# Kernel optimization log

Measured on AMD Instinct MI355X. Metric: run time of the kernel, lower is better.

## Reference

```python
import jax, jax.numpy as jnp
import numpy as np

N_E = 8192
E_DIM = 256
BETA = 0.25


def setup_inputs() -> dict:
    key = jax.random.key(0)
    k_z, k_w = jax.random.split(key)
    z = jax.random.normal(k_z, (32, E_DIM, 32, 32), dtype=jnp.float32)
    # nn.Embedding weight init: uniform(-1/n_e, 1/n_e)
    W = jax.random.uniform(k_w, (N_E, E_DIM), dtype=jnp.float32,
                           minval=-1.0 / N_E, maxval=1.0 / N_E)
    return {"z": z, "W": W}


def reference(z, W):
    B, C, H, Wd = z.shape
    beta = jnp.float32(BETA)
    z_nhwc = jnp.transpose(z, (0, 2, 3, 1))          # (B,H,W,C)
    zf = z_nhwc.reshape(-1, C)                       # (N,C)
    # squared-distance matrix (N, n_e)
    d = (jnp.sum(zf * zf, axis=1, keepdims=True)
         + jnp.sum(W * W, axis=1)
         - 2.0 * jnp.matmul(zf, W.T))
    idx = jnp.argmin(d, axis=1)                      # (N,)
    # one-hot @ W == gather
    z_q = W[idx].reshape(z_nhwc.shape)               # (B,H,W,C)
    loss = (jnp.mean((jax.lax.stop_gradient(z_q) - z_nhwc) ** 2)
            + beta * jnp.mean((z_q - jax.lax.stop_gradient(z_nhwc)) ** 2))
    # straight-through estimator
    z_q = z_nhwc + jax.lax.stop_gradient(z_q - z_nhwc)
    # codebook usage perplexity
    n = idx.shape[0]
    e_mean = jnp.zeros((N_E,), jnp.float32).at[idx].add(1.0) / n
    perplexity = jnp.exp(-jnp.sum(e_mean * jnp.log(e_mean + 1e-10)))
    z_q = jnp.transpose(z_q, (0, 3, 1, 2))           # back to (B,C,H,W)
    index = idx.reshape(B, H, Wd)
    return z_q, loss, index, perplexity
```

## Files before the change

kernel.cpp:

```cpp
#include <hip/hip_runtime.h>
#include <float.h>
#include <math.h>

#define OUT_LOSS 8388608
#define OUT_IDX  8388609
#define OUT_PERP 8421377

#define WS_ZH    0ull
#define WS_ZL    16777216ull
#define WS_ZT    0ull
#define WS_WH    33554432ull
#define WS_S     37748736ull
#define WS_B     37879808ull
#define WS_MAXW  37912576ull
#define WS_IDX   37912640ull
#define WS_HIST  38043712ull
#define WS_CAND  38076480ull
#define WS_FULL  38469696ull
#define WS_FKEY  38600768ull
#define WS_CNT   38862912ull
#define WS_LOSS  38862920ull
#define WS_WL    38866944ull

typedef short v8s __attribute__((ext_vector_type(8)));
typedef float v4f __attribute__((ext_vector_type(4)));

__device__ __forceinline__ unsigned short bf16rne(float f) {
  unsigned u = __float_as_uint(f);
  return (unsigned short)((u + 0x7FFFu + ((u >> 16) & 1u)) >> 16);
}
__device__ __forceinline__ float bf16tof(unsigned short h) {
  return __uint_as_float(((unsigned)h) << 16);
}

__device__ __forceinline__ void gl_lds16(const void* g, void* l) {
  __builtin_amdgcn_global_load_lds(
      (const __attribute__((address_space(1))) unsigned int*)g,
      (__attribute__((address_space(3))) unsigned int*)l, 16, 0, 0);
}

__global__ void k_zero(int* __restrict__ hist, unsigned long long* __restrict__ fkey,
                       int* __restrict__ cnt, double* __restrict__ loss,
                       unsigned* __restrict__ maxw) {
  const int i = blockIdx.x * 256 + threadIdx.x;
  if (i < 8192) hist[i] = 0;
  else if (i < 40960) fkey[i - 8192] = ~0ull;
  else if (i == 40960) cnt[0] = 0;
  else if (i == 40961) cnt[1] = 0;
  else if (i == 40962) *loss = 0.0;
  else if (i == 40963) *maxw = 0u;
}

__global__ __launch_bounds__(256) void k_split(const float* __restrict__ W,
                                               unsigned short* __restrict__ Wh,
                                               unsigned short* __restrict__ Wl) {
  const int u = blockIdx.x * 256 + threadIdx.x;
  const int kc = u >> 15, grp = (u >> 6) & 511, q = (u >> 4) & 3, col = u & 15;
  const int j = grp * 16 + col, k0 = kc * 32 + q * 8;
  const float4 w0 = *(const float4*)(W + (size_t)j * 256 + k0);
  const float4 w1 = *(const float4*)(W + (size_t)j * 256 + k0 + 4);
  const float wv[8] = {w0.x, w0.y, w0.z, w0.w, w1.x, w1.y, w1.z, w1.w};
  unsigned short h[8] __attribute__((aligned(16)));
  unsigned short l[8] __attribute__((aligned(16)));
#pragma unroll
  for (int i = 0; i < 8; ++i) {
    h[i] = bf16rne(wv[i]);
    l[i] = bf16rne(__fsub_rn(wv[i], bf16tof(h[i])));
  }
  *(uint4*)(Wh + (size_t)u * 8) = *(const uint4*)h;
  *(uint4*)(Wl + (size_t)u * 8) = *(const uint4*)l;
}

__global__ __launch_bounds__(256) void k_splitz(const float* __restrict__ z,
    unsigned short* __restrict__ Zh, unsigned short* __restrict__ Zl) {
  const int gt = blockIdx.x * 256 + threadIdx.x;
  const int kc = gt >> 15;
  const int n  = gt & 32767;
  const int b = n >> 10, p = n & 1023;
  const float* zp = z + (size_t)b * 262144 + (size_t)(kc * 32) * 1024 + p;
  unsigned short hh[32] __attribute__((aligned(16)));
  unsigned short ll[32] __attribute__((aligned(16)));
#pragma unroll
  for (int i = 0; i < 32; ++i) {
    const float v = zp[(size_t)i * 1024];
    const unsigned short h = bf16rne(v);
    hh[i] = h;
    ll[i] = bf16rne(__fsub_rn(v, bf16tof(h)));
  }
  const size_t o = (size_t)kc * 1048576 + (size_t)(n >> 4) * 512 + (size_t)(n & 15) * 8;
#pragma unroll
  for (int q = 0; q < 4; ++q) *(uint4*)(Zh + o + q * 128) = *(const uint4*)(hh + q * 8);
#pragma unroll
  for (int q = 0; q < 4; ++q) *(uint4*)(Zl + o + q * 128) = *(const uint4*)(ll + q * 8);
}

__global__ __launch_bounds__(256) void k_zt(const float* __restrict__ z,
                                            float* __restrict__ zT) {
  const int gt = blockIdx.x * 256 + threadIdx.x;
  const int kc = gt >> 15;
  const int n  = gt & 32767;
  const int b = n >> 10, p = n & 1023;
  const float* zp = z + (size_t)b * 262144 + (size_t)(kc * 32) * 1024 + p;
  float v[32] __attribute__((aligned(16)));
#pragma unroll
  for (int i = 0; i < 32; ++i) v[i] = zp[(size_t)i * 1024];
  float* dst = zT + (size_t)n * 256 + kc * 32;
#pragma unroll
  for (int j = 0; j < 8; ++j) *(float4*)(dst + j * 4) = *(const float4*)(v + j * 4);
}

__device__ __forceinline__ float np_sumsq256(const float* __restrict__ base,
                                             const int stride) {
  float h[2];
#pragma unroll
  for (int half = 0; half < 2; ++half) {
    const float* a = base + (size_t)(half * 128) * stride;
    float r[8];
#pragma unroll
    for (int k = 0; k < 8; ++k) { const float v = a[(size_t)k * stride]; r[k] = __fmul_rn(v, v); }
    for (int i = 8; i < 128; i += 8) {
#pragma unroll
      for (int k = 0; k < 8; ++k) {
        const float v = a[(size_t)(i + k) * stride];
        r[k] = __fadd_rn(r[k], __fmul_rn(v, v));
      }
    }
    h[half] = __fadd_rn(
        __fadd_rn(__fadd_rn(r[0], r[1]), __fadd_rn(r[2], r[3])),
        __fadd_rn(__fadd_rn(r[4], r[5]), __fadd_rn(r[6], r[7])));
  }
  return __fadd_rn(h[0], h[1]);
}

__global__ __launch_bounds__(256) void k_sz(const float* __restrict__ z,
                                            float* __restrict__ S) {
  const int n = blockIdx.x * 256 + threadIdx.x;
  S[n] = np_sumsq256(z + (size_t)(n >> 10) * 262144 + (n & 1023), 1024);
}

__global__ __launch_bounds__(256) void k_wsq(const float* __restrict__ W,
                                             float* __restrict__ B,
                                             unsigned* __restrict__ maxw) {
  const int j = blockIdx.x * 256 + threadIdx.x;
  const float b = np_sumsq256(W + (size_t)j * 256, 1);
  B[j] = b;
  atomicMax(maxw, __float_as_uint(b));
}

__device__ __forceinline__ void merge5(float& a1, int& ai1, float& a2, int& ai2,
                                       float& a3, float b1, int bi1, float b2,
                                       int bi2, float b3) {
  const bool t1 = (b1 < a1) || (b1 == a1 && bi1 < ai1);
  const float w2v = t1 ? b2 : a2; const int w2i = t1 ? bi2 : ai2;
  const float w3v = t1 ? b3 : a3;
  const float l1v = t1 ? a1 : b1; const int l1i = t1 ? ai1 : bi1;
  const float l2v = t1 ? a2 : b2;
  const float n1v = t1 ? b1 : a1; const int n1i = t1 ? bi1 : ai1;
  const bool t2 = (w2v < l1v) || (w2v == l1v && w2i < l1i);
  a1 = n1v; ai1 = n1i;
  a2 = t2 ? w2v : l1v; ai2 = t2 ? w2i : l1i;
  a3 = t2 ? fminf(w3v, l1v) : fminf(w2v, l2v);
}

#define AL_OFF   0
#define BH0_OFF  32768
#define BH1_OFF  65536
#define BL0_OFF  98304
#define BL1_OFF  131072
#define SC_OFF   32768
#define SMEM_SZ  163840
__global__ __launch_bounds__(512, 1) void k_main(
    const unsigned short* __restrict__ Zh, const unsigned short* __restrict__ Zl,
    const unsigned short* __restrict__ Wh, const unsigned short* __restrict__ Wl,
    const float* __restrict__ S, const float* __restrict__ B,
    const unsigned* __restrict__ maxw, int* __restrict__ idxb,
    int* __restrict__ cand, int* __restrict__ full, int* __restrict__ cnt) {
  extern __shared__ __align__(16) char smem[];
  const int t = threadIdx.x;
  const int w = t >> 6, lane = t & 63, col = lane & 15, q = lane >> 4;
  const int phalf = w >> 2, strip = w & 3;
  const int n0 = blockIdx.x << 6;

  float spx[8];
#pragma unroll
  for (int s = 0; s < 8; ++s)
    spx[s] = S[n0 + phalf * 32 + (s >> 2) * 16 + q * 4 + (s & 3)];

  v8s ah[8][2];
  const size_t abase = (size_t)(n0 >> 4) * 512 + (size_t)lane * 8;
#pragma unroll
  for (int kc = 0; kc < 8; ++kc)
#pragma unroll
    for (int pt = 0; pt < 2; ++pt)
      ah[kc][pt] = *(const v8s*)(Zh + (size_t)kc * 1048576 + abase
                                 + (size_t)(phalf * 2 + pt) * 512);

  {
    const size_t ab = (size_t)w * 1048576 + abase;
    char* dl = smem + AL_OFF + w * 4096;
#pragma unroll
    for (int i = 0; i < 4; ++i) gl_lds16(Zl + ab + (size_t)i * 512, dl + i * 1024);
  }
  {
    const size_t bb = (size_t)(w * 4) * 512 + (size_t)lane * 8;
#pragma unroll
    for (int i = 0; i < 4; ++i)
      gl_lds16(Wh + bb + (size_t)i * 512, smem + BH0_OFF + (w * 4 + i) * 1024);
#pragma unroll
    for (int i = 0; i < 4; ++i)
      gl_lds16(Wl + bb + (size_t)i * 512, smem + BL0_OFF + (w * 4 + i) * 1024);
  }
  __syncthreads();

  float m1[8], m2[8], m3[8]; int i1[8], i2[8];
#pragma unroll
  for (int s = 0; s < 8; ++s) {
    m1[s] = FLT_MAX; m2[s] = FLT_MAX; m3[s] = FLT_MAX;
    i1[s] = 0x7fffffff; i2[s] = 0x7fffffff;
  }

  v4f acc[2][8];
#pragma unroll
  for (int pt = 0; pt < 2; ++pt)
#pragma unroll
    for (int nt = 0; nt < 8; ++nt) acc[pt][nt] = (v4f){0.f, 0.f, 0.f, 0.f};

  for (int ct = 0; ct < 16; ++ct) {
#pragma unroll
    for (int kc = 0; kc < 8; ++kc) {
      const int it = ct * 8 + kc;
      if (it < 127) {
        const int nc = it + 1;
        const size_t cb = (size_t)(nc & 7) * 262144 + (size_t)(nc >> 3) * 16384
                        + (size_t)(w * 4) * 512 + (size_t)lane * 8;
        char* nh = smem + ((nc & 1) ? BH1_OFF : BH0_OFF) + (w * 4) * 1024;
        char* nl = smem + ((nc & 1) ? BL1_OFF : BL0_OFF) + (w * 4) * 1024;
#pragma unroll
        for (int i = 0; i < 4; ++i)
          gl_lds16(Wh + cb + (size_t)i * 512, nh + i * 1024);
#pragma unroll
        for (int i = 0; i < 4; ++i)
          gl_lds16(Wl + cb + (size_t)i * 512, nl + i * 1024);
      }
      const char* bhb = smem + ((it & 1) ? BH1_OFF : BH0_OFF);
      const char* blb = smem + ((it & 1) ? BL1_OFF : BL0_OFF);
      v8s al[2];
#pragma unroll
      for (int pt = 0; pt < 2; ++pt)
        al[pt] = *(const v8s*)(smem + AL_OFF + kc * 4096
                               + (phalf * 2 + pt) * 1024 + lane * 16);
#pragma unroll
      for (int nt = 0; nt < 8; ++nt) {
        const v8s bh = *(const v8s*)(bhb + (strip * 8 + nt) * 1024 + lane * 16);
        const v8s bl = *(const v8s*)(blb + (strip * 8 + nt) * 1024 + lane * 16);
#pragma unroll
        for (int pt = 0; pt < 2; ++pt) {
          acc[pt][nt] = __builtin_amdgcn_mfma_f32_16x16x32_bf16(ah[kc][pt], bh, acc[pt][nt], 0, 0, 0);
          acc[pt][nt] = __builtin_amdgcn_mfma_f32_16x16x32_bf16(al[pt], bh, acc[pt][nt], 0, 0, 0);
          acc[pt][nt] = __builtin_amdgcn_mfma_f32_16x16x32_bf16(ah[kc][pt], bl, acc[pt][nt], 0, 0, 0);
        }
      }
      __syncthreads();
      if (kc == 7) {
#pragma unroll
        for (int nt = 0; nt < 8; ++nt) {
          const int code = ct * 512 + strip * 128 + nt * 16 + col;
          const float bb = B[code];
#pragma unroll
          for (int pt = 0; pt < 2; ++pt) {
            const v4f a = acc[pt][nt];
#pragma unroll
            for (int r = 0; r < 4; ++r) {
              const int s = pt * 4 + r;
              const float d = __fsub_rn(__fadd_rn(spx[s], bb), __fmul_rn(2.f, a[r]));
              const bool c1 = (d < m1[s]);
              const bool c2 = (d < m2[s]);
              const bool c3 = (d < m3[s]);
              m3[s] = c2 ? m2[s] : (c3 ? d : m3[s]);
              m2[s] = c1 ? m1[s] : (c2 ? d : m2[s]);
              i2[s] = c1 ? i1[s] : (c2 ? code : i2[s]);
              m1[s] = c1 ? d : m1[s];
              i1[s] = c1 ? code : i1[s];
            }
          }
#pragma unroll
          for (int pt = 0; pt < 2; ++pt) acc[pt][nt] = (v4f){0.f, 0.f, 0.f, 0.f};
        }
      }
    }
  }

#pragma unroll
  for (int s = 0; s < 8; ++s) {
    for (int msk = 1; msk < 16; msk <<= 1) {
      const float b1 = __shfl_xor(m1[s], msk, 16);
      const int  bi1 = __shfl_xor(i1[s], msk, 16);
      const float b2 = __shfl_xor(m2[s], msk, 16);
      const int  bi2 = __shfl_xor(i2[s], msk, 16);
      const float b3 = __shfl_xor(m3[s], msk, 16);
      merge5(m1[s], i1[s], m2[s], i2[s], m3[s], b1, bi1, b2, bi2, b3);
    }
  }
  __syncthreads();
  float* sc = (float*)(smem + SC_OFF);
  if (col == 0) {
#pragma unroll
    for (int s = 0; s < 8; ++s) {
      const int px = phalf * 32 + (s >> 2) * 16 + q * 4 + (s & 3);
      const int base = (px * 4 + strip) * 5;
      sc[base]     = m1[s];
      sc[base + 1] = __int_as_float(i1[s]);
      sc[base + 2] = m2[s];
      sc[base + 3] = __int_as_float(i2[s]);
      sc[base + 4] = m3[s];
    }
  }
  __syncthreads();
  if (t < 64) {
    const int base0 = t * 20;
    float A1 = sc[base0], A2 = sc[base0 + 2], A3 = sc[base0 + 4];
    int AI1 = __float_as_int(sc[base0 + 1]), AI2 = __float_as_int(sc[base0 + 3]);
    for (int st = 1; st < 4; ++st) {
      const int base = base0 + st * 5;
      merge5(A1, AI1, A2, AI2, A3, sc[base], __float_as_int(sc[base + 1]),
             sc[base + 2], __float_as_int(sc[base + 3]), sc[base + 4]);
    }
    const int n = n0 + t;
    idxb[n] = AI1;
    const float nw = sqrtf(S[n]) * sqrtf(__uint_as_float(*maxw));
    const float win = 2.0f * (1.52587890625e-05f * nw + 1e-6f)
                    + 2.0f * ldexpf(1.0f, ilogbf(fmaxf(A1, 1e-30f)) - 23);
    if (A2 <= A1 + win) {
      if (A3 <= A1 + win) {
        const int p = atomicAdd(&cnt[1], 1);
        full[p] = n;
      } else {
        const int p = atomicAdd(&cnt[0], 1);
        cand[3 * p] = n; cand[3 * p + 1] = AI1; cand[3 * p + 2] = AI2;
      }
    }
  }
}

__global__ __launch_bounds__(256) void k_cand(const float* __restrict__ zT,
    const float* __restrict__ W, const float* __restrict__ S,
    const float* __restrict__ B, const int* __restrict__ cand,
    const int* __restrict__ cnt, int* __restrict__ idxb) {
  const int e = blockIdx.x * 256 + threadIdx.x;
  if (e >= cnt[0]) return;
  const int n = cand[3 * e], ca = cand[3 * e + 1], cb = cand[3 * e + 2];
  const float* zp = zT + (size_t)n * 256;
  const float* wa = W + (size_t)ca * 256;
  const float* wb = W + (size_t)cb * 256;
  float a1 = 0.f, a2 = 0.f;
  for (int c = 0; c < 256; ++c) {
    const float zv = zp[c];
    a1 = __builtin_fmaf(zv, wa[c], a1);
    a2 = __builtin_fmaf(zv, wb[c], a2);
  }
  const float d1 = __fsub_rn(__fadd_rn(S[n], B[ca]), __fmul_rn(2.f, a1));
  const float d2 = __fsub_rn(__fadd_rn(S[n], B[cb]), __fmul_rn(2.f, a2));
  idxb[n] = (d1 < d2) ? ca : ((d2 < d1) ? cb : min(ca, cb));
}

__global__ __launch_bounds__(256) void k_full(const float* __restrict__ zT,
    const float* __restrict__ W, const float* __restrict__ S,
    const float* __restrict__ B, const int* __restrict__ full,
    const int* __restrict__ cnt, unsigned long long* __restrict__ fkey) {
  extern __shared__ __align__(16) char fsm[];
  float* zsf = (float*)fsm;
  float* wt  = (float*)(fsm + 32768);
  float* mv  = (float*)(fsm + 32768 + 32896);
  int*   mi  = (int*)(fsm + 32768 + 32896 + 4224);
  const int t = threadIdx.x;
  const int pg = t & 7, cg = t >> 3;
  const int fN = min(cnt[1], 32768);
  const int units = ((fN + 31) >> 5) << 5;
  for (int e = blockIdx.x; e < units; e += 2048) {
    const int g = e >> 5, tt = e & 31;
    const int c0 = tt << 8;
    __syncthreads();
    {
      const int px = t >> 3, c8 = t & 7;
      const int f = (g << 5) + px;
      const int n = (f < fN) ? full[f] : full[0];
      const float4* src = (const float4*)(zT + (size_t)n * 256 + c8 * 32);
      const int colq = (((px >> 2) ^ c8) << 2) + (px & 3);
#pragma unroll
      for (int j = 0; j < 8; ++j) {
        const float4 v = src[j];
        const int c = c8 * 32 + j * 4;
        zsf[(c    ) * 32 + colq] = v.x;
        zsf[(c + 1) * 32 + colq] = v.y;
        zsf[(c + 2) * 32 + colq] = v.z;
        zsf[(c + 3) * 32 + colq] = v.w;
      }
    }
    float s4[4];
#pragma unroll
    for (int i = 0; i < 4; ++i) {
      const int f = (g << 5) + (pg << 2) + i;
      s4[i] = (f < fN) ? S[full[f]] : 0.f;
    }
    float bm[4]; int bj[4];
#pragma unroll
    for (int i = 0; i < 4; ++i) { bm[i] = FLT_MAX; bj[i] = 0x7fffffff; }
    float acc[4][8];
#pragma unroll
    for (int i = 0; i < 4; ++i)
#pragma unroll
      for (int u = 0; u < 8; ++u) acc[i][u] = 0.f;
    for (int kc = 0; kc < 8; ++kc) {
      const int kb = kc << 5;
      __syncthreads();
#pragma unroll
      for (int p = 0; p < 8; ++p) {
        const int jl = (t >> 3) + (p << 5);
        const float4 wv4 =
            *(const float4*)&W[(size_t)(c0 + jl) * 256 + kb + ((t & 7) << 2)];
        const int k0 = (t & 7) << 2;
        wt[(k0    ) * 257 + jl] = wv4.x;
        wt[(k0 + 1) * 257 + jl] = wv4.y;
        wt[(k0 + 2) * 257 + jl] = wv4.z;
        wt[(k0 + 3) * 257 + jl] = wv4.w;
      }
      __syncthreads();
      const int zq = ((pg ^ kc) & 7) << 2;
      for (int k = 0; k < 32; ++k) {
        const float4 z4 = *(const float4*)&zsf[(kb + k) * 32 + zq];
        const float4 wA = *(const float4*)&wt[k * 257 + (cg << 3)];
        const float4 wB = *(const float4*)&wt[k * 257 + (cg << 3) + 4];
        const float zv[4] = {z4.x, z4.y, z4.z, z4.w};
        const float wv[8] = {wA.x, wA.y, wA.z, wA.w, wB.x, wB.y, wB.z, wB.w};
#pragma unroll
        for (int i = 0; i < 4; ++i)
#pragma unroll
          for (int u = 0; u < 8; ++u)
            acc[i][u] = __builtin_fmaf(zv[i], wv[u], acc[i][u]);
      }
    }
#pragma unroll
    for (int u = 0; u < 8; ++u) {
      const int code = c0 + (cg << 3) + u;
      const float bb = B[code];
#pragma unroll
      for (int i = 0; i < 4; ++i) {
        const float d = __fsub_rn(__fadd_rn(s4[i], bb), __fmul_rn(2.f, acc[i][u]));
        if (d < bm[i]) { bm[i] = d; bj[i] = code; }
      }
    }
    __syncthreads();
#pragma unroll
    for (int i = 0; i < 4; ++i) {
      const int px = (pg << 2) + i;
      mv[px * 33 + cg] = bm[i];
      mi[px * 33 + cg] = bj[i];
    }
    __syncthreads();
    if (t < 32) {
      float m = mv[t * 33]; int j = mi[t * 33];
      for (int c = 1; c < 32; ++c) {
        const float v = mv[t * 33 + c]; const int vi = mi[t * 33 + c];
        if (v < m || (v == m && vi < j)) { m = v; j = vi; }
      }
      const int f = (g << 5) + t;
      if (f < fN) {
        const unsigned long long key =
            (((unsigned long long)__float_as_uint(m)) << 13) | (unsigned)j;
        atomicMin(&fkey[f], key);
      }
    }
  }
}

__global__ __launch_bounds__(256) void k_fullfin(const int* __restrict__ full,
    const int* __restrict__ cnt, const unsigned long long* __restrict__ fkey,
    int* __restrict__ idxb) {
  const int f = blockIdx.x * 256 + threadIdx.x;
  if (f < cnt[1]) idxb[full[f]] = (int)(fkey[f] & 8191ull);
}

__global__ __launch_bounds__(256) void k_zq(const float* __restrict__ z,
    const float* __restrict__ W, const int* __restrict__ idxb,
    float* __restrict__ out, double* __restrict__ loss, int* __restrict__ hist) {
  __shared__ float red[256];
  const int t = threadIdx.x;
  const int tx = t & 63, ty = t >> 6;
  const int n0 = blockIdx.x << 6;
  const int n = n0 + tx;
  const int b = n >> 10;
  const int p = n & 1023;
  const int myidx = idxb[n];
  const float* wrow = W + (size_t)myidx * 256;
  float lsum = 0.f;
#pragma unroll 4
  for (int cc = 0; cc < 64; ++cc) {
    const int c = ty * 64 + cc;
    const float qv = wrow[c];
    const size_t off = (size_t)b * 262144 + (size_t)c * 1024 + p;
    const float zv = z[off];
    const float d = __fsub_rn(qv, zv);
    lsum = __builtin_fmaf(d, d, lsum);
    out[off] = __fadd_rn(zv, d);
  }
  red[t] = lsum;
  __syncthreads();
  for (int o = 128; o > 0; o >>= 1) {
    if (t < o) red[t] += red[t + o];
    __syncthreads();
  }
  if (t == 0) atomicAdd(loss, (double)red[0]);
  if (ty == 0) atomicAdd(&hist[myidx], 1);
  if (ty == 1) out[OUT_IDX + n] = (float)myidx;
}

__global__ void k_final(const int* __restrict__ hist,
                        const double* __restrict__ loss,
                        float* __restrict__ out) {
  __shared__ double sh[256];
  const int t = threadIdx.x;
  double s = 0.0;
  for (int j = t; j < 8192; j += 256) {
    const double e = (double)hist[j] / 32768.0;
    s += e * log(e + 1e-10);
  }
  sh[t] = s;
  __syncthreads();
  for (int off = 128; off > 0; off >>= 1) {
    if (t < off) sh[t] += sh[t + off];
    __syncthreads();
  }
  if (t == 0) {
    out[OUT_PERP] = (float)exp(-sh[0]);
    out[OUT_LOSS] = (float)(1.25 * (*loss) / 8388608.0);
  }
}

extern "C" void kernel_launch(void* const* d_in, const int* in_sizes, int n_in,
                              void* d_out, int out_size, void* d_ws, size_t ws_size,
                              hipStream_t stream) {
  const float* z = (const float*)d_in[0];
  const float* W = (const float*)d_in[1];
  float* out = (float*)d_out;
  char* ws = (char*)d_ws;
  unsigned short* Zh = (unsigned short*)(ws + WS_ZH);
  unsigned short* Zl = (unsigned short*)(ws + WS_ZL);
  unsigned short* Wh = (unsigned short*)(ws + WS_WH);
  unsigned short* Wl = (unsigned short*)(ws + WS_WL);
  float*  zT   = (float*)(ws + WS_ZT);
  float*  S    = (float*)(ws + WS_S);
  float*  B    = (float*)(ws + WS_B);
  unsigned* maxw = (unsigned*)(ws + WS_MAXW);
  int*    idxb = (int*)(ws + WS_IDX);
  int*    hist = (int*)(ws + WS_HIST);
  int*    cand = (int*)(ws + WS_CAND);
  int*    full = (int*)(ws + WS_FULL);
  unsigned long long* fkey = (unsigned long long*)(ws + WS_FKEY);
  int*    cnt  = (int*)(ws + WS_CNT);
  double* loss = (double*)(ws + WS_LOSS);

  hipLaunchKernelGGL(k_zero,    dim3(161),  dim3(256), 0, stream, hist, fkey, cnt, loss, maxw);
  hipLaunchKernelGGL(k_split,   dim3(1024), dim3(256), 0, stream, W, Wh, Wl);
  hipLaunchKernelGGL(k_splitz,  dim3(1024), dim3(256), 0, stream, z, Zh, Zl);
  hipLaunchKernelGGL(k_sz,      dim3(128),  dim3(256), 0, stream, z, S);
  hipLaunchKernelGGL(k_wsq,     dim3(32),   dim3(256), 0, stream, W, B, maxw);
  hipLaunchKernelGGL(k_main,    dim3(512),  dim3(512), SMEM_SZ, stream,
                     Zh, Zl, Wh, Wl, S, B, maxw, idxb, cand, full, cnt);
  hipLaunchKernelGGL(k_zt,      dim3(1024), dim3(256), 0, stream, z, zT);
  hipLaunchKernelGGL(k_cand,    dim3(128),  dim3(256), 0, stream, zT, W, S, B, cand, cnt, idxb);
  hipLaunchKernelGGL(k_full,    dim3(2048), dim3(256), 74112, stream, zT, W, S, B, full, cnt, fkey);
  hipLaunchKernelGGL(k_fullfin, dim3(128),  dim3(256), 0, stream, full, cnt, fkey, idxb);
  hipLaunchKernelGGL(k_zq,      dim3(512),  dim3(256), 0, stream, z, W, idxb, out, loss, hist);
  hipLaunchKernelGGL(k_final,   dim3(1),    dim3(256), 0, stream, hist, loss, out);
}
```

Baseline: 834.1 us.

## Stage Z-high tile in LDS and stream W-low fragments via registers

Moves the high half of the Z tile from registers into LDS alongside the low half. Replaces the double-buffered LDS staging of the W low part with direct per-wave global loads into registers, prefetched one iteration ahead. Shared memory shrinks from 160KB to 128KB and register pressure from the 16 held A fragments drops. In exchange each wave issues redundant global loads for W-low (strips shared across the two pixel-half waves), and the prefetch latency is exposed inside the MFMA loop.

After: 795.7 us. -4.6%, faster.

```diff
diff --git a/kernel.cpp b/kernel.cpp
--- a/kernel.cpp
+++ b/kernel.cpp
@@ -162,13 +162,12 @@
   a3 = t2 ? fminf(w3v, l1v) : fminf(w2v, l2v);
 }
 
-#define AL_OFF   0
-#define BH0_OFF  32768
-#define BH1_OFF  65536
-#define BL0_OFF  98304
-#define BL1_OFF  131072
-#define SC_OFF   32768
-#define SMEM_SZ  163840
+#define AH_OFF   0
+#define AL_OFF   32768
+#define B0_OFF   65536
+#define B1_OFF   98304
+#define SC_OFF   65536
+#define SMEM_SZ  131072
 __global__ __launch_bounds__(512, 1) void k_main(
     const unsigned short* __restrict__ Zh, const unsigned short* __restrict__ Zl,
     const unsigned short* __restrict__ Wh, const unsigned short* __restrict__ Wl,
@@ -186,18 +185,12 @@
   for (int s = 0; s < 8; ++s)
     spx[s] = S[n0 + phalf * 32 + (s >> 2) * 16 + q * 4 + (s & 3)];
 
-  v8s ah[8][2];
-  const size_t abase = (size_t)(n0 >> 4) * 512 + (size_t)lane * 8;
-#pragma unroll
-  for (int kc = 0; kc < 8; ++kc)
-#pragma unroll
-    for (int pt = 0; pt < 2; ++pt)
-      ah[kc][pt] = *(const v8s*)(Zh + (size_t)kc * 1048576 + abase
-                                 + (size_t)(phalf * 2 + pt) * 512);
-
   {
-    const size_t ab = (size_t)w * 1048576 + abase;
+    const size_t ab = (size_t)w * 1048576 + (size_t)(n0 >> 4) * 512 + (size_t)lane * 8;
+    char* dh = smem + AH_OFF + w * 4096;
     char* dl = smem + AL_OFF + w * 4096;
+#pragma unroll
+    for (int i = 0; i < 4; ++i) gl_lds16(Zh + ab + (size_t)i * 512, dh + i * 1024);
 #pragma unroll
     for (int i = 0; i < 4; ++i) gl_lds16(Zl + ab + (size_t)i * 512, dl + i * 1024);
   }
@@ -205,10 +198,13 @@
     const size_t bb = (size_t)(w * 4) * 512 + (size_t)lane * 8;
 #pragma unroll
     for (int i = 0; i < 4; ++i)
-      gl_lds16(Wh + bb + (size_t)i * 512, smem + BH0_OFF + (w * 4 + i) * 1024);
-#pragma unroll
-    for (int i = 0; i < 4; ++i)
-      gl_lds16(Wl + bb + (size_t)i * 512, smem + BL0_OFF + (w * 4 + i) * 1024);
+      gl_lds16(Wh + bb + (size_t)i * 512, smem + B0_OFF + (w * 4 + i) * 1024);
+  }
+  v8s bl[8];
+  {
+    const unsigned short* p = Wl + (size_t)(strip * 8) * 512 + (size_t)lane * 8;
+#pragma unroll
+    for (int nt = 0; nt < 8; ++nt) bl[nt] = *(const v8s*)(p + nt * 512);
   }
   __syncthreads();
 
@@ -233,32 +229,34 @@
         const int nc = it + 1;
         const size_t cb = (size_t)(nc & 7) * 262144 + (size_t)(nc >> 3) * 16384
                         + (size_t)(w * 4) * 512 + (size_t)lane * 8;
-        char* nh = smem + ((nc & 1) ? BH1_OFF : BH0_OFF) + (w * 4) * 1024;
-        char* nl = smem + ((nc & 1) ? BL1_OFF : BL0_OFF) + (w * 4) * 1024;
+        char* nh = smem + ((nc & 1) ? B1_OFF : B0_OFF) + (w * 4) * 1024;
 #pragma unroll
         for (int i = 0; i < 4; ++i)
           gl_lds16(Wh + cb + (size_t)i * 512, nh + i * 1024);
-#pragma unroll
-        for (int i = 0; i < 4; ++i)
-          gl_lds16(Wl + cb + (size_t)i * 512, nl + i * 1024);
-      }
-      const char* bhb = smem + ((it & 1) ? BH1_OFF : BH0_OFF);
-      const char* blb = smem + ((it & 1) ? BL1_OFF : BL0_OFF);
-      v8s al[2];
-#pragma unroll
-      for (int pt = 0; pt < 2; ++pt)
-        al[pt] = *(const v8s*)(smem + AL_OFF + kc * 4096
-                               + (phalf * 2 + pt) * 1024 + lane * 16);
+      }
+      const char* bhb = smem + ((it & 1) ? B1_OFF : B0_OFF);
+      const int nc2 = (it + 1) & 127;
+      const unsigned short* blsrc = Wl + (size_t)(nc2 & 7) * 262144
+                                  + (size_t)(nc2 >> 3) * 16384
+                                  + (size_t)(strip * 8) * 512 + (size_t)lane * 8;
+      v8s ah[2], al[2];
+#pragma unroll
+      for (int pt = 0; pt < 2; ++pt) {
+        const int g = phalf * 2 + pt;
+        ah[pt] = *(const v8s*)(smem + AH_OFF + kc * 4096 + g * 1024 + lane * 16);
+        al[pt] = *(const v8s*)(smem + AL_OFF + kc * 4096 + g * 1024 + lane * 16);
+      }
 #pragma unroll
       for (int nt = 0; nt < 8; ++nt) {
         const v8s bh = *(const v8s*)(bhb + (strip * 8 + nt) * 1024 + lane * 16);
-        const v8s bl = *(const v8s*)(blb + (strip * 8 + nt) * 1024 + lane * 16);
+        const v8s blv = bl[nt];
 #pragma unroll
         for (int pt = 0; pt < 2; ++pt) {
-          acc[pt][nt] = __builtin_amdgcn_mfma_f32_16x16x32_bf16(ah[kc][pt], bh, acc[pt][nt], 0, 0, 0);
+          acc[pt][nt] = __builtin_amdgcn_mfma_f32_16x16x32_bf16(ah[pt], bh, acc[pt][nt], 0, 0, 0);
           acc[pt][nt] = __builtin_amdgcn_mfma_f32_16x16x32_bf16(al[pt], bh, acc[pt][nt], 0, 0, 0);
-          acc[pt][nt] = __builtin_amdgcn_mfma_f32_16x16x32_bf16(ah[kc][pt], bl, acc[pt][nt], 0, 0, 0);
+          acc[pt][nt] = __builtin_amdgcn_mfma_f32_16x16x32_bf16(ah[pt], blv, acc[pt][nt], 0, 0, 0);
         }
+        bl[nt] = *(const v8s*)(blsrc + nt * 512);
       }
       __syncthreads();
       if (kc == 7) {
```
